# Optimization experiments

Measured on AMD Instinct MI355X. Metric: run time of the kernel, lower is better.

Reference implementation:

```python
import jax, jax.numpy as jnp
import numpy as np
from jax import lax


def _lin_weights(in_size, out_size):
    # torch F.interpolate(mode='bilinear', align_corners=False) source indices
    scale = in_size / out_size
    src = (jnp.arange(out_size, dtype=jnp.float32) + 0.5) * scale - 0.5
    src = jnp.maximum(src, 0.0)
    i0 = jnp.minimum(jnp.floor(src).astype(jnp.int32), in_size - 1)
    i1 = jnp.minimum(i0 + 1, in_size - 1)
    w = src - i0.astype(jnp.float32)
    return i0, i1, w


def bilinear_resize(x, out_h, out_w):
    # x: (..., H, W) -> (..., out_h, out_w), separable bilinear
    H, W = x.shape[-2], x.shape[-1]
    i0, i1, wh = _lin_weights(H, out_h)
    j0, j1, ww = _lin_weights(W, out_w)
    x = x[..., i0, :] * (1.0 - wh)[:, None] + x[..., i1, :] * wh[:, None]
    x = x[..., :, j0] * (1.0 - ww) + x[..., :, j1] * ww
    return x


def setup_inputs() -> dict:
    key = jax.random.key(0)
    ks = jax.random.split(key, 16)
    b, H, W = 16, 56, 56
    n = H * W
    dim, heads, dh, agent_num = 512, 8, 64, 49
    ID = heads * dh  # inner_dim == dim
    s = 0.02
    return {
        'x': jax.random.normal(ks[0], (b, n, dim), jnp.float32),
        'H': H, 'W': W,
        'q_w': s * jax.random.normal(ks[1], (dim, ID), jnp.float32),
        'q_b': s * jax.random.normal(ks[2], (ID,), jnp.float32),
        'kv_w': s * jax.random.normal(ks[3], (dim, 2 * ID), jnp.float32),
        'kv_b': s * jax.random.normal(ks[4], (2 * ID,), jnp.float32),
        'proj_w': s * jax.random.normal(ks[5], (ID, dim), jnp.float32),
        'proj_b': s * jax.random.normal(ks[6], (dim,), jnp.float32),
        'dwc_w': s * jax.random.normal(ks[7], (ID, 1, 3, 3), jnp.float32),
        'dwc_b': s * jax.random.normal(ks[8], (ID,), jnp.float32),
        'an_bias': s * jax.random.normal(ks[9], (heads, agent_num, 7, 7), jnp.float32),
        'na_bias': s * jax.random.normal(ks[10], (heads, agent_num, 7, 7), jnp.float32),
        'ah_bias': s * jax.random.normal(ks[11], (1, heads, agent_num, H, 1), jnp.float32),
        'aw_bias': s * jax.random.normal(ks[12], (1, heads, agent_num, 1, W), jnp.float32),
        'ha_bias': s * jax.random.normal(ks[13], (1, heads, H, 1, agent_num), jnp.float32),
        'wa_bias': s * jax.random.normal(ks[14], (1, heads, 1, W, agent_num), jnp.float32),
    }


def reference(x, H, W, q_w, q_b, kv_w, kv_b, proj_w, proj_b, dwc_w, dwc_b,
              an_bias, na_bias, ah_bias, aw_bias, ha_bias, wa_bias):
    b, n, c = x.shape
    heads, agent_num = an_bias.shape[0], an_bias.shape[1]
    ID = q_w.shape[1]
    dh = ID // heads
    scale = dh ** -0.5
    pool = int(round(agent_num ** 0.5))  # 7

    q = x @ q_w + q_b                      # (b, n, ID)
    kv = x @ kv_w + kv_b                   # (b, n, 2*ID)  (sr_ratio == 1)
    k, v = kv[..., :ID], kv[..., ID:]

    # adaptive avg pool of q on the (H, W) grid -> agent tokens (b, agent_num, ID)
    qi = q.reshape(b, pool, H // pool, pool, W // pool, ID)
    agent = qi.mean(axis=(2, 4)).reshape(b, agent_num, ID)

    qh = q.reshape(b, n, heads, dh).transpose(0, 2, 1, 3)          # (b,h,n,d)
    kh = k.reshape(b, n, heads, dh).transpose(0, 2, 1, 3)
    vh = v.reshape(b, n, heads, dh).transpose(0, 2, 1, 3)
    ah = agent.reshape(b, agent_num, heads, dh).transpose(0, 2, 1, 3)  # (b,h,a,d)

    # stage 1: agent tokens attend to k/v, with interpolated + factored position bias
    pb1 = bilinear_resize(an_bias, H, W).reshape(1, heads, agent_num, n)
    pb2 = (ah_bias + aw_bias).reshape(1, heads, agent_num, n)
    s1 = jnp.einsum('bhad,bhnd->bhan', ah * scale, kh) + pb1 + pb2
    agent_attn = jax.nn.softmax(s1, axis=-1)                        # (b,h,a,n)
    agent_v = jnp.einsum('bhan,bhnd->bhad', agent_attn, vh)         # (b,h,a,d)

    # stage 2: queries attend to agent tokens
    ab1 = bilinear_resize(na_bias, H, W).reshape(1, heads, agent_num, n).transpose(0, 1, 3, 2)
    ab2 = (ha_bias + wa_bias).reshape(1, heads, n, agent_num)
    s2 = jnp.einsum('bhnd,bhad->bhna', qh * scale, ah) + ab1 + ab2
    q_attn = jax.nn.softmax(s2, axis=-1)                            # (b,h,n,a)
    out = jnp.einsum('bhna,bhad->bhnd', q_attn, agent_v)
    out = out.transpose(0, 2, 1, 3).reshape(b, n, ID)

    # depthwise 3x3 conv over v as spatial residual
    v_img = v.reshape(b, H, W, ID).transpose(0, 3, 1, 2)            # (b,ID,H,W)
    dwc = lax.conv_general_dilated(v_img, dwc_w, (1, 1), 'SAME',
                                   feature_group_count=ID,
                                   dimension_numbers=('NCHW', 'OIHW', 'NCHW'))
    dwc = dwc + dwc_b[None, :, None, None]
    out = out + dwc.transpose(0, 2, 3, 1).reshape(b, n, ID)

    return out @ proj_w + proj_b
```

## Files before the change

### kernel.cpp

```cpp
#include <hip/hip_runtime.h>
#include <hip/hip_bf16.h>

#define DEV __device__ __forceinline__

typedef __attribute__((ext_vector_type(4))) float f32x4;
typedef __attribute__((ext_vector_type(8))) short bf8_t;
typedef __attribute__((ext_vector_type(4))) unsigned int u32x4;

static constexpr float QSCALE = 0.125f;

DEV float bflo(unsigned int w){ union{unsigned int i; float f;} x; x.i = w << 16; return x.f; }
DEV float bfhi(unsigned int w){ union{unsigned int i; float f;} x; x.i = w & 0xffff0000u; return x.f; }
DEV float bf2f(unsigned short u){ union{unsigned int i; float f;} x; x.i = ((unsigned int)u) << 16; return x.f; }
DEV unsigned short f2bf(float f){
  union{float f; unsigned int i;} x; x.f = f;
  unsigned int i = x.i;
  i += 0x7fffu + ((i >> 16) & 1u);
  return (unsigned short)(i >> 16);
}
DEV unsigned int pack2(float a, float b){ return (unsigned int)f2bf(a) | ((unsigned int)f2bf(b) << 16); }

DEV void mfma_acc(f32x4& c, const bf8_t& a, const bf8_t& b){
  asm volatile("v_mfma_f32_16x16x32_bf16 %0, %1, %2, %0" : "+v"(c) : "v"(a), "v"(b));
}

DEV void cp16(unsigned short* l, const unsigned short* g){
  __builtin_amdgcn_global_load_lds(
      (const __attribute__((address_space(1))) unsigned int*)(const void*)g,
      (__attribute__((address_space(3))) unsigned int*)(void*)l, 16, 0, 0);
}

DEV float wred_max(float v){
  #pragma unroll
  for (int m = 1; m < 64; m <<= 1) v = fmaxf(v, __shfl_xor(v, m));
  return v;
}
DEV float wred_sum(float v){
  #pragma unroll
  for (int m = 1; m < 64; m <<= 1) v += __shfl_xor(v, m);
  return v;
}

__global__ void k_prep(const float* __restrict__ qw, const float* __restrict__ kvw,
                       const float* __restrict__ pw, const float* __restrict__ qb,
                       const float* __restrict__ kvb,
                       unsigned short* __restrict__ wqkvt, unsigned short* __restrict__ wprojt,
                       float* __restrict__ qkvbias){
  const int i0 = blockIdx.x * blockDim.x + threadIdx.x;
  const int stride = gridDim.x * blockDim.x;
  for (int idx = i0; idx < 1536*512; idx += stride){
    int n = idx >> 9, k = idx & 511;
    float v = (n < 512) ? qw[k*512 + n] : kvw[k*1024 + (n - 512)];
    wqkvt[idx] = f2bf(v);
  }
  for (int idx = i0; idx < 512*512; idx += stride){
    int n = idx >> 9, k = idx & 511;
    wprojt[idx] = f2bf(pw[k*512 + n]);
  }
  for (int idx = i0; idx < 1536; idx += stride)
    qkvbias[idx] = (idx < 512) ? qb[idx] : kvb[idx - 512];
}

__global__ void k_cvt_x(const float* __restrict__ x, unsigned short* __restrict__ xb){
  const long total8 = (long)50176*512/8;
  for (long i = (long)blockIdx.x*blockDim.x + threadIdx.x; i < total8; i += (long)gridDim.x*blockDim.x){
    const float4* p = (const float4*)(x + i*8);
    float4 a = p[0], b = p[1];
    u32x4 o;
    o.x = pack2(a.x, a.y); o.y = pack2(a.z, a.w);
    o.z = pack2(b.x, b.y); o.w = pack2(b.z, b.w);
    *(u32x4*)(xb + i*8) = o;
  }
}

template<bool OUT_BF>
__global__ __launch_bounds__(256) void k_gemm(const unsigned short* __restrict__ A,
    const unsigned short* __restrict__ Bt, const float* __restrict__ bias,
    void* __restrict__ Cp, const int N, const int nxb){
  __shared__ unsigned short Al[128][64];
  __shared__ unsigned short Bl[128][64];
  const int tid = threadIdx.x, lane = tid & 63, w = tid >> 6;
  const int bid = blockIdx.x;
  const int cxd = bid & 7, kk = bid >> 3;
  const int yi = kk / nxb, xb = kk - yi*nxb;
  const int m0 = (cxd + 8*yi) * 128, n0 = xb * 128;
  const int wr = (w >> 1) * 64, wc = (w & 1) * 64;
  const int fr = lane & 15, kg = lane >> 4;

  const int lr = lane >> 3, slog = (lane & 7) ^ lr;
  const unsigned short* gA = A  + (size_t)(m0 + w*32 + lr)*512 + slog*8;
  const unsigned short* gB = Bt + (size_t)(n0 + w*32 + lr)*512 + slog*8;

  f32x4 acc[4][4] = {};
  for (int kt = 0; kt < 8; ++kt){
    const int k0 = kt * 64;
    __syncthreads();
    #pragma unroll
    for (int cch = 0; cch < 4; ++cch){
      cp16(&Al[w*32 + cch*8][0], gA + (size_t)cch*8*512 + k0);
      cp16(&Bl[w*32 + cch*8][0], gB + (size_t)cch*8*512 + k0);
    }
    __syncthreads();
    bf8_t afl[4], afh[4];
    #pragma unroll
    for (int i = 0; i < 4; ++i){
      const int row = wr + i*16 + fr;
      const int sl = (kg ^ (row & 7)) * 8;
      afl[i] = *(const bf8_t*)&Al[row][sl];
      afh[i] = *(const bf8_t*)&Al[row][sl ^ 32];
    }
    #pragma unroll
    for (int j = 0; j < 4; ++j){
      const int row = wc + j*16 + fr;
      const int sl = (kg ^ (row & 7)) * 8;
      bf8_t bfl = *(const bf8_t*)&Bl[row][sl];
      bf8_t bfh = *(const bf8_t*)&Bl[row][sl ^ 32];
      #pragma unroll
      for (int i = 0; i < 4; ++i){
        mfma_acc(acc[i][j], afl[i], bfl);
        mfma_acc(acc[i][j], afh[i], bfh);
      }
    }
  }
  const int rb = kg * 4;
  #pragma unroll
  for (int j = 0; j < 4; ++j){
    const int col = n0 + wc + j*16 + fr;
    const float bs = bias[col];
    #pragma unroll
    for (int i = 0; i < 4; ++i){
      #pragma unroll
      for (int r = 0; r < 4; ++r){
        const int row = m0 + wr + i*16 + rb + r;
        float v = acc[i][j][r] + bs;
        if (OUT_BF) ((unsigned short*)Cp)[(size_t)row*N + col] = f2bf(v);
        else        ((float*)Cp)[(size_t)row*N + col] = v;
      }
    }
  }
}

__global__ void k_pool(const unsigned short* __restrict__ qkv, float* __restrict__ agent){
  const int b = blockIdx.x / 49, a = blockIdx.x % 49;
  const int p1 = a / 7, p2 = a % 7;
  for (int c = threadIdx.x; c < 512; c += 256){
    float s = 0.f;
    for (int r = 0; r < 8; ++r)
      for (int cc = 0; cc < 8; ++cc){
        int pix = (p1*8 + r)*56 + p2*8 + cc;
        s += bf2f(qkv[((size_t)b*3136 + pix)*1536 + c]);
      }
    agent[((size_t)b*49 + a)*512 + c] = s * (1.0f/64.0f);
  }
}

DEV void lin_w(int o, int& i0, int& i1, float& w){
  float src = (o + 0.5f)*0.125f - 0.5f;
  src = fmaxf(src, 0.f);
  int f = (int)floorf(src);
  i0 = min(f, 6); i1 = min(i0 + 1, 6); w = src - (float)i0;
}

__global__ void k_bias(const float* __restrict__ an, const float* __restrict__ ahb,
                       const float* __restrict__ awb,
                       const float* __restrict__ na, const float* __restrict__ hab,
                       const float* __restrict__ wab,
                       float* __restrict__ pbs, float* __restrict__ absumP){
  const int tot1 = 8*49*3136;
  for (int idx = blockIdx.x*blockDim.x + threadIdx.x; idx < tot1; idx += gridDim.x*blockDim.x){
    int n = idx % 3136, ha = idx / 3136;
    int y = n / 56, x = n % 56;
    int iy0, iy1, ix0, ix1; float wy, wx;
    lin_w(y, iy0, iy1, wy); lin_w(x, ix0, ix1, wx);
    const float* t = an + (size_t)ha*49;
    float v0 = t[iy0*7+ix0]*(1.f-wy) + t[iy1*7+ix0]*wy;
    float v1 = t[iy0*7+ix1]*(1.f-wy) + t[iy1*7+ix1]*wy;
    float v = v0*(1.f-wx) + v1*wx;
    pbs[idx] = v + ahb[ha*56 + y] + awb[ha*56 + x];
  }
  const int tot2 = 8*3136*64;
  for (int idx = blockIdx.x*blockDim.x + threadIdx.x; idx < tot2; idx += gridDim.x*blockDim.x){
    int a = idx & 63, hn = idx >> 6;
    int n = hn % 3136, h = hn / 3136;
    float out = 0.f;
    if (a < 49){
      int y = n / 56, x = n % 56;
      int iy0, iy1, ix0, ix1; float wy, wx;
      lin_w(y, iy0, iy1, wy); lin_w(x, ix0, ix1, wx);
      const float* t = na + (size_t)(h*49 + a)*49;
      float v0 = t[iy0*7+ix0]*(1.f-wy) + t[iy1*7+ix0]*wy;
      float v1 = t[iy0*7+ix1]*(1.f-wy) + t[iy1*7+ix1]*wy;
      float v = v0*(1.f-wx) + v1*wx;
      out = v + hab[(h*56+y)*49 + a] + wab[(h*56+x)*49 + a];
    }
    absumP[idx] = out;
  }
}

__global__ __launch_bounds__(256) void k_attn1(const unsigned short* __restrict__ qkv,
    const float* __restrict__ agent, const float* __restrict__ pbs,
    float* __restrict__ pacc, float* __restrict__ pml){
  const int bi = blockIdx.x;
  const int sp = bi % 7, h = (bi/7) & 7, b = bi / 56;
  const int tid = threadIdx.x, lane = tid & 63, w = tid >> 6;
  const int c = lane & 15, kg = lane >> 4;

  __shared__ unsigned short ag[64][72];
  __shared__ unsigned short Kl[64][72];
  __shared__ unsigned short Vt[64][72];
  __shared__ unsigned short Pl[4][16][72];

  for (int it = tid; it < 64*8; it += 256){
    int a = it >> 3, o = it & 7;
    u32x4 wv = {0,0,0,0};
    if (a < 49){
      const float* p = agent + ((size_t)b*49 + a)*512 + h*64 + o*8;
      f32x4 lo = *(const f32x4*)p, hi = *(const f32x4*)(p+4);
      wv.x = pack2(lo.x*QSCALE, lo.y*QSCALE);
      wv.y = pack2(lo.z*QSCALE, lo.w*QSCALE);
      wv.z = pack2(hi.x*QSCALE, hi.y*QSCALE);
      wv.w = pack2(hi.z*QSCALE, hi.w*QSCALE);
    }
    *(u32x4*)&ag[a][o*8] = wv;
  }
  __syncthreads();
  bf8_t agf[2];
  agf[0] = *(const bf8_t*)&ag[w*16 + c][kg*8];
  agf[1] = *(const bf8_t*)&ag[w*16 + c][kg*8 + 32];

  const int aw = w*16 + c;
  const int amin = aw < 49 ? aw : 48;
  const bool areal = aw < 49;
  const float* pbrow = pbs + ((size_t)(h*49 + amin))*3136 + sp*448;

  float m_ = -1e30f, l_ = 0.f;
  f32x4 acc[4] = {};

  for (int t = 0; t < 7; ++t){
    const int gn0 = sp*448 + t*64;
    f32x4 pb4[4];
    #pragma unroll
    for (int i = 0; i < 4; ++i)
      pb4[i] = *(const f32x4*)(pbrow + t*64 + 16*i + 4*kg);

    __syncthreads();
    #pragma unroll
    for (int ii = 0; ii < 2; ++ii){
      int it = tid + ii*256;
      int pix = it >> 3, o = it & 7;
      const unsigned short* kp = qkv + ((size_t)b*3136 + gn0 + pix)*1536 + 512 + h*64 + o*8;
      *(u32x4*)&Kl[pix][o*8] = *(const u32x4*)kp;
    }
    #pragma unroll
    for (int ii = 0; ii < 2; ++ii){
      int it = tid + ii*256;
      int pix = it & 63, o = it >> 6;
      const unsigned short* vp = qkv + ((size_t)b*3136 + gn0 + pix)*1536 + 1024 + h*64 + o*8;
      u32x4 vv = *(const u32x4*)vp;
      unsigned int vals[4] = {vv.x, vv.y, vv.z, vv.w};
      #pragma unroll
      for (int q = 0; q < 4; ++q){
        Vt[o*8 + 2*q][pix]     = (unsigned short)(vals[q] & 0xffffu);
        Vt[o*8 + 2*q + 1][pix] = (unsigned short)(vals[q] >> 16);
      }
    }
    __syncthreads();

    f32x4 sa[4] = {};
    #pragma unroll
    for (int i = 0; i < 4; ++i){
      bf8_t kf0 = *(const bf8_t*)&Kl[i*16 + c][kg*8];
      bf8_t kf1 = *(const bf8_t*)&Kl[i*16 + c][kg*8 + 32];
      mfma_acc(sa[i], kf0, agf[0]);
      mfma_acc(sa[i], kf1, agf[1]);
    }

    float s16[4][4]; float mx = -1e30f;
    #pragma unroll
    for (int i = 0; i < 4; ++i)
      #pragma unroll
      for (int r = 0; r < 4; ++r){
        float sv = areal ? (sa[i][r] + pb4[i][r]) : -1e30f;
        s16[i][r] = sv; mx = fmaxf(mx, sv);
      }
    mx = fmaxf(mx, __shfl_xor(mx, 16));
    mx = fmaxf(mx, __shfl_xor(mx, 32));
    float mn = fmaxf(m_, mx);
    float al = __expf(m_ - mn);
    float rs = 0.f;
    #pragma unroll
    for (int i = 0; i < 4; ++i)
      #pragma unroll
      for (int r = 0; r < 4; ++r){
        float p = __expf(s16[i][r] - mn);
        s16[i][r] = p; rs += p;
      }
    rs += __shfl_xor(rs, 16);
    rs += __shfl_xor(rs, 32);
    m_ = mn; l_ = l_*al + rs;

    #pragma unroll
    for (int i = 0; i < 4; ++i){
      uint2 pw;
      pw.x = pack2(s16[i][0], s16[i][1]);
      pw.y = pack2(s16[i][2], s16[i][3]);
      *(uint2*)&Pl[w][c][16*i + 4*kg] = pw;
    }

    float al_s[4];
    #pragma unroll
    for (int r = 0; r < 4; ++r) al_s[r] = __shfl(al, 4*kg + r);
    #pragma unroll
    for (int j = 0; j < 4; ++j)
      #pragma unroll
      for (int r = 0; r < 4; ++r) acc[j][r] *= al_s[r];

    bf8_t pf0 = *(const bf8_t*)&Pl[w][c][kg*8];
    bf8_t pf1 = *(const bf8_t*)&Pl[w][c][kg*8 + 32];
    #pragma unroll
    for (int j = 0; j < 4; ++j){
      bf8_t vf0 = *(const bf8_t*)&Vt[j*16 + c][kg*8];
      bf8_t vf1 = *(const bf8_t*)&Vt[j*16 + c][kg*8 + 32];
      mfma_acc(acc[j], pf0, vf0);
      mfma_acc(acc[j], pf1, vf1);
    }
  }

  const int base = ((b*8 + h)*7 + sp)*49;
  #pragma unroll
  for (int r = 0; r < 4; ++r){
    const int a = w*16 + 4*kg + r;
    if (a < 49){
      float* dst = pacc + (size_t)(base + a)*64 + c;
      #pragma unroll
      for (int j = 0; j < 4; ++j) dst[16*j] = acc[j][r];
    }
  }
  if (kg == 0 && areal){
    pml[(base + aw)*2]     = m_;
    pml[(base + aw)*2 + 1] = l_;
  }
}

__global__ void k_merge(const float* __restrict__ pacc, const float* __restrict__ pml,
                        float* __restrict__ agentv){
  const int gw = blockIdx.x*4 + (threadIdx.x >> 6);
  const int lane = threadIdx.x & 63;
  if (gw >= 16*8*49) return;
  const int a = gw % 49, bh = gw / 49;
  float ms[7], ls[7], M = -1e30f;
  #pragma unroll
  for (int s = 0; s < 7; ++s){
    int base = (bh*7 + s)*49 + a;
    ms[s] = pml[base*2]; ls[s] = pml[base*2 + 1];
    M = fmaxf(M, ms[s]);
  }
  float L = 0.f, o = 0.f;
  #pragma unroll
  for (int s = 0; s < 7; ++s){
    float e = __expf(ms[s] - M);
    L += ls[s]*e;
    o += pacc[(size_t)((bh*7 + s)*49 + a)*64 + lane]*e;
  }
  agentv[(size_t)(bh*49 + a)*64 + lane] = o / L;
}

__global__ __launch_bounds__(256) void k_attn2(const unsigned short* __restrict__ qkv,
    const float* __restrict__ agent, const float* __restrict__ agentv,
    const float* __restrict__ absumP, unsigned short* __restrict__ outb){
  const int blk = blockIdx.x;
  const int bh = blk / 13, tloc = blk % 13;
  const int b = bh >> 3, h = bh & 7;
  const int tid = threadIdx.x, lane = tid & 63, w = tid >> 6;
  const int c = lane & 15, kg = lane >> 4;

  __shared__ unsigned short ag[64][72];
  __shared__ unsigned short avT[64][72];
  __shared__ unsigned short Pl[4][16][72];

  for (int it = tid; it < 64*8; it += 256){
    int a = it >> 3, o = it & 7;
    u32x4 wv = {0,0,0,0};
    if (a < 49){
      const float* p = agent + ((size_t)b*49 + a)*512 + h*64 + o*8;
      f32x4 lo = *(const f32x4*)p, hi = *(const f32x4*)(p+4);
      wv.x = pack2(lo.x*QSCALE, lo.y*QSCALE);
      wv.y = pack2(lo.z*QSCALE, lo.w*QSCALE);
      wv.z = pack2(hi.x*QSCALE, hi.y*QSCALE);
      wv.w = pack2(hi.z*QSCALE, hi.w*QSCALE);
    }
    *(u32x4*)&ag[a][o*8] = wv;
  }
  for (int it = tid; it < 64*64; it += 256){
    int a = it >> 6, d = it & 63;
    avT[d][a] = (a < 49) ? f2bf(agentv[((size_t)bh*49 + a)*64 + d]) : (unsigned short)0;
  }
  __syncthreads();

  const int ti = tloc*4 + w;
  if (ti >= 49) return;
  const int pix0 = ti*64;

  bf8_t af[4][2];
  #pragma unroll
  for (int i = 0; i < 4; ++i){
    af[i][0] = *(const bf8_t*)&ag[i*16 + c][kg*8];
    af[i][1] = *(const bf8_t*)&ag[i*16 + c][kg*8 + 32];
  }

  for (int j = 0; j < 4; ++j){
    const int pix = pix0 + 16*j + c;
    const unsigned short* qp = qkv + ((size_t)b*3136 + pix)*1536 + h*64;
    bf8_t qf0 = *(const bf8_t*)(qp + kg*8);
    bf8_t qf1 = *(const bf8_t*)(qp + kg*8 + 32);
    f32x4 sa[4] = {};
    #pragma unroll
    for (int i = 0; i < 4; ++i){
      mfma_acc(sa[i], af[i][0], qf0);
      mfma_acc(sa[i], af[i][1], qf1);
    }
    const float* bp = absumP + ((size_t)h*3136 + pix)*64 + 4*kg;
    f32x4 bias4[4];
    #pragma unroll
    for (int i = 0; i < 4; ++i) bias4[i] = *(const f32x4*)(bp + 16*i);
    float s16[4][4]; float mx = -1e30f;
    #pragma unroll
    for (int i = 0; i < 4; ++i){
      #pragma unroll
      for (int r = 0; r < 4; ++r){
        int a = 16*i + 4*kg + r;
        float sv = (a < 49) ? (sa[i][r] + bias4[i][r]) : -1e30f;
        s16[i][r] = sv; mx = fmaxf(mx, sv);
      }
    }
    mx = fmaxf(mx, __shfl_xor(mx, 16));
    mx = fmaxf(mx, __shfl_xor(mx, 32));
    float rs = 0.f;
    #pragma unroll
    for (int i = 0; i < 4; ++i){
      #pragma unroll
      for (int r = 0; r < 4; ++r){
        float p = __expf(s16[i][r] - mx);
        s16[i][r] = p; rs += p;
      }
    }
    rs += __shfl_xor(rs, 16);
    rs += __shfl_xor(rs, 32);
    #pragma unroll
    for (int i = 0; i < 4; ++i){
      uint2 pw;
      pw.x = pack2(s16[i][0], s16[i][1]);
      pw.y = pack2(s16[i][2], s16[i][3]);
      *(uint2*)&Pl[w][c][16*i + 4*kg] = pw;
    }
    bf8_t pf0 = *(const bf8_t*)&Pl[w][c][kg*8];
    bf8_t pf1 = *(const bf8_t*)&Pl[w][c][kg*8 + 32];
    f32x4 acc[4] = {};
    #pragma unroll
    for (int jd = 0; jd < 4; ++jd){
      bf8_t vf0 = *(const bf8_t*)&avT[jd*16 + c][kg*8];
      bf8_t vf1 = *(const bf8_t*)&avT[jd*16 + c][kg*8 + 32];
      mfma_acc(acc[jd], pf0, vf0);
      mfma_acc(acc[jd], pf1, vf1);
    }
    float l_s[4];
    #pragma unroll
    for (int r = 0; r < 4; ++r) l_s[r] = __shfl(rs, 4*kg + r);
    #pragma unroll
    for (int r = 0; r < 4; ++r){
      const int prow = pix0 + 16*j + 4*kg + r;
      unsigned short* op = outb + ((size_t)b*3136 + prow)*512 + h*64;
      float inv = 1.0f / l_s[r];
      #pragma unroll
      for (int jd = 0; jd < 4; ++jd)
        op[jd*16 + c] = f2bf(acc[jd][r] * inv);
    }
  }
}

__global__ __launch_bounds__(256) void k_dwc(const unsigned short* __restrict__ qkv,
    const float* __restrict__ dwcw, const float* __restrict__ dwcb,
    unsigned short* __restrict__ outb){
  const int tid = threadIdx.x;
  const int oct = tid & 63, pxl = tid >> 6;
  const int bid = blockIdx.x;
  const int gp4 = (bid & 7) * 1568 + (bid >> 3);
  const int gp = gp4 * 4 + pxl;
  const int b = gp / 3136, pix = gp - b*3136;
  const int y = pix / 56, x = pix - y*56;
  const int c0 = oct * 8;

  f32x4 w4[18];
  const f32x4* wp = (const f32x4*)(dwcw + c0*9);
  #pragma unroll
  for (int i = 0; i < 18; ++i) w4[i] = wp[i];
  #define W(j,t) (w4[((j)*9+(t)) >> 2][((j)*9+(t)) & 3])

  float o[8];
  {
    f32x4 b0 = *(const f32x4*)(dwcb + c0);
    f32x4 b1 = *(const f32x4*)(dwcb + c0 + 4);
    o[0]=b0.x; o[1]=b0.y; o[2]=b0.z; o[3]=b0.w;
    o[4]=b1.x; o[5]=b1.y; o[6]=b1.z; o[7]=b1.w;
  }

  const unsigned short* vbase = qkv + (size_t)b*3136*1536 + 1024 + c0;
  #pragma unroll
  for (int ky = 0; ky < 3; ++ky){
    const int ny = y + ky - 1;
    if ((unsigned)ny >= 56u) continue;
    #pragma unroll
    for (int kx = 0; kx < 3; ++kx){
      const int nx = x + kx - 1;
      if ((unsigned)nx >= 56u) continue;
      u32x4 vv = *(const u32x4*)(vbase + (size_t)(ny*56 + nx)*1536);
      const int t = ky*3 + kx;
      o[0] += W(0,t)*bflo(vv.x); o[1] += W(1,t)*bfhi(vv.x);
      o[2] += W(2,t)*bflo(vv.y); o[3] += W(3,t)*bfhi(vv.y);
      o[4] += W(4,t)*bflo(vv.z); o[5] += W(5,t)*bfhi(vv.z);
      o[6] += W(6,t)*bflo(vv.w); o[7] += W(7,t)*bfhi(vv.w);
    }
  }
  #undef W

  unsigned short* op = outb + (size_t)gp*512 + c0;
  u32x4 a = *(u32x4*)op;
  o[0] += bflo(a.x); o[1] += bfhi(a.x);
  o[2] += bflo(a.y); o[3] += bfhi(a.y);
  o[4] += bflo(a.z); o[5] += bfhi(a.z);
  o[6] += bflo(a.w); o[7] += bfhi(a.w);
  u32x4 r;
  r.x = pack2(o[0], o[1]); r.y = pack2(o[2], o[3]);
  r.z = pack2(o[4], o[5]); r.w = pack2(o[6], o[7]);
  *(u32x4*)op = r;
}

extern "C" void kernel_launch(void* const* d_in, const int* in_sizes, int n_in,
                              void* d_out, int out_size, void* d_ws, size_t ws_size,
                              hipStream_t stream){
  const float* x       = (const float*)d_in[0];
  const float* q_w     = (const float*)d_in[3];
  const float* q_b     = (const float*)d_in[4];
  const float* kv_w    = (const float*)d_in[5];
  const float* kv_b    = (const float*)d_in[6];
  const float* proj_w  = (const float*)d_in[7];
  const float* proj_b  = (const float*)d_in[8];
  const float* dwc_w   = (const float*)d_in[9];
  const float* dwc_b   = (const float*)d_in[10];
  const float* an_bias = (const float*)d_in[11];
  const float* na_bias = (const float*)d_in[12];
  const float* ah_bias = (const float*)d_in[13];
  const float* aw_bias = (const float*)d_in[14];
  const float* ha_bias = (const float*)d_in[15];
  const float* wa_bias = (const float*)d_in[16];

  char* ws = (char*)d_ws;
  size_t off = 0;
  auto alloc = [&](size_t bytes) -> void* {
    void* p = ws + off;
    off += (bytes + 255) & ~(size_t)255;
    return p;
  };
  unsigned short* xb     = (unsigned short*)alloc((size_t)50176*512*2);
  unsigned short* qkv    = (unsigned short*)alloc((size_t)50176*1536*2);
  unsigned short* wqkvt  = (unsigned short*)alloc((size_t)1536*512*2);
  unsigned short* wprojt = (unsigned short*)alloc((size_t)512*512*2);
  float* qkvb   = (float*)alloc((size_t)1536*4);
  float* agent  = (float*)alloc((size_t)16*49*512*4);
  float* agentv = (float*)alloc((size_t)16*8*49*64*4);
  float* pbs    = (float*)alloc((size_t)8*49*3136*4);
  float* absumP = (float*)alloc((size_t)8*3136*64*4);
  float* pacc   = (float*)alloc((size_t)16*8*8*49*64*4);
  float* pml    = (float*)alloc((size_t)16*8*8*49*2*4);
  unsigned short* outb = (unsigned short*)alloc((size_t)50176*512*2);
  if (off > ws_size) return;

  k_prep<<<512, 256, 0, stream>>>(q_w, kv_w, proj_w, q_b, kv_b, wqkvt, wprojt, qkvb);
  k_cvt_x<<<2048, 256, 0, stream>>>(x, xb);
  k_gemm<true><<<4704, 256, 0, stream>>>(xb, wqkvt, qkvb, qkv, 1536, 12);
  k_pool<<<784, 256, 0, stream>>>(qkv, agent);
  k_bias<<<1024, 256, 0, stream>>>(an_bias, ah_bias, aw_bias, na_bias, ha_bias, wa_bias, pbs, absumP);
  k_attn1<<<896, 256, 0, stream>>>(qkv, agent, pbs, pacc, pml);
  k_merge<<<1568, 256, 0, stream>>>(pacc, pml, agentv);
  k_attn2<<<1664, 256, 0, stream>>>(qkv, agent, agentv, absumP, outb);
  k_dwc<<<12544, 256, 0, stream>>>(qkv, dwc_w, dwc_b, outb);
  k_gemm<false><<<1568, 256, 0, stream>>>(outb, wprojt, proj_b, d_out, 512, 4);
}
```

Measured before the change: 363.7 us.

## Vectorize agent pooling and use direct-to-LDS swizzled K loads in attention

k_pool now has each thread sum two adjacent channels with 32-bit loads instead of scalar 16-bit loads. In k_attn1 the K tile is loaded with cp16 (async global-to-LDS copy) into an unpadded XOR-swizzled layout, and the MFMA fragment reads apply the matching swizzle. The V transpose now pairs lanes via shuffle to write 32-bit words instead of 16-bit scalar LDS stores. The aim is to cut load and LDS store instruction counts and bank conflicts; correctness depends on the swizzle matching cp16's per-lane layout.

```diff
diff --git a/kernel.cpp b/kernel.cpp
--- a/kernel.cpp
+++ b/kernel.cpp
@@ -143,15 +143,19 @@
 __global__ void k_pool(const unsigned short* __restrict__ qkv, float* __restrict__ agent){
   const int b = blockIdx.x / 49, a = blockIdx.x % 49;
   const int p1 = a / 7, p2 = a % 7;
-  for (int c = threadIdx.x; c < 512; c += 256){
-    float s = 0.f;
-    for (int r = 0; r < 8; ++r)
-      for (int cc = 0; cc < 8; ++cc){
-        int pix = (p1*8 + r)*56 + p2*8 + cc;
-        s += bf2f(qkv[((size_t)b*3136 + pix)*1536 + c]);
-      }
-    agent[((size_t)b*49 + a)*512 + c] = s * (1.0f/64.0f);
-  }
+  const int c0 = threadIdx.x * 2;
+  float s0 = 0.f, s1 = 0.f;
+  const unsigned short* base = qkv + (size_t)b*3136*1536 + c0;
+  for (int r = 0; r < 8; ++r)
+    #pragma unroll
+    for (int cc = 0; cc < 8; ++cc){
+      int pix = (p1*8 + r)*56 + p2*8 + cc;
+      unsigned int v = *(const unsigned int*)(base + (size_t)pix*1536);
+      s0 += bflo(v); s1 += bfhi(v);
+    }
+  float* dst = agent + ((size_t)b*49 + a)*512 + c0;
+  dst[0] = s0 * (1.0f/64.0f);
+  dst[1] = s1 * (1.0f/64.0f);
 }
 
 DEV void lin_w(int o, int& i0, int& i1, float& w){
@@ -206,7 +210,7 @@
   const int c = lane & 15, kg = lane >> 4;
 
   __shared__ unsigned short ag[64][72];
-  __shared__ unsigned short Kl[64][72];
+  __shared__ unsigned short Kl[64][64];
   __shared__ unsigned short Vt[64][72];
   __shared__ unsigned short Pl[4][16][72];
 
@@ -233,6 +237,9 @@
   const bool areal = aw < 49;
   const float* pbrow = pbs + ((size_t)(h*49 + amin))*3136 + sp*448;
 
+  const int lr = lane >> 3, slog = (lane & 7) ^ lr;
+  const unsigned short* gK = qkv + ((size_t)b*3136 + sp*448 + w*16 + lr)*1536 + 512 + h*64 + slog*8;
+
   float m_ = -1e30f, l_ = 0.f;
   f32x4 acc[4] = {};
 
@@ -244,24 +251,24 @@
       pb4[i] = *(const f32x4*)(pbrow + t*64 + 16*i + 4*kg);
 
     __syncthreads();
+    cp16(&Kl[w*16][0],     gK + (size_t)t*64*1536);
+    cp16(&Kl[w*16 + 8][0], gK + (size_t)(t*64 + 8)*1536);
     #pragma unroll
     for (int ii = 0; ii < 2; ++ii){
-      int it = tid + ii*256;
-      int pix = it >> 3, o = it & 7;
-      const unsigned short* kp = qkv + ((size_t)b*3136 + gn0 + pix)*1536 + 512 + h*64 + o*8;
-      *(u32x4*)&Kl[pix][o*8] = *(const u32x4*)kp;
-    }
-    #pragma unroll
-    for (int ii = 0; ii < 2; ++ii){
-      int it = tid + ii*256;
-      int pix = it & 63, o = it >> 6;
-      const unsigned short* vp = qkv + ((size_t)b*3136 + gn0 + pix)*1536 + 1024 + h*64 + o*8;
+      const int o = w + ii*4;
+      const unsigned short* vp = qkv + ((size_t)b*3136 + gn0 + lane)*1536 + 1024 + h*64 + o*8;
       u32x4 vv = *(const u32x4*)vp;
-      unsigned int vals[4] = {vv.x, vv.y, vv.z, vv.w};
+      unsigned int own[4] = {vv.x, vv.y, vv.z, vv.w};
+      const int colbase = lane & ~1;
+      const bool odd = lane & 1;
       #pragma unroll
       for (int q = 0; q < 4; ++q){
-        Vt[o*8 + 2*q][pix]     = (unsigned short)(vals[q] & 0xffffu);
-        Vt[o*8 + 2*q + 1][pix] = (unsigned short)(vals[q] >> 16);
+        unsigned int par = __shfl_xor(own[q], 1);
+        unsigned int wv;
+        int drow;
+        if (!odd){ wv = (own[q] & 0xffffu) | (par << 16);          drow = o*8 + 2*q; }
+        else     { wv = (par >> 16) | (own[q] & 0xffff0000u);      drow = o*8 + 2*q + 1; }
+        *(unsigned int*)&Vt[drow][colbase] = wv;
       }
     }
     __syncthreads();
@@ -269,8 +276,10 @@
     f32x4 sa[4] = {};
     #pragma unroll
     for (int i = 0; i < 4; ++i){
-      bf8_t kf0 = *(const bf8_t*)&Kl[i*16 + c][kg*8];
-      bf8_t kf1 = *(const bf8_t*)&Kl[i*16 + c][kg*8 + 32];
+      const int row = i*16 + c;
+      const int sl = (kg ^ (row & 7)) * 8;
+      bf8_t kf0 = *(const bf8_t*)&Kl[row][sl];
+      bf8_t kf1 = *(const bf8_t*)&Kl[row][sl ^ 32];
       mfma_acc(sa[i], kf0, agf[0]);
       mfma_acc(sa[i], kf1, agf[1]);
     }
```

Measured after the change: 367.3 us. About the same (+1.0%).
